# Performance work log

Measured on AMD Instinct MI355X. Metric: run time of the kernel, lower is better.

Reference implementation:

```python
import jax, jax.numpy as jnp
import numpy as np

B, F, H, M, T = 4096, 256, 256, 3, 30
IN0 = 2 + F  # GRU layer-0 input: concat(current_pos[2], context[F])


def setup_inputs() -> dict:
    key = jax.random.key(0)
    ks = jax.random.split(key, 15)
    s = 0.05
    rn = lambda k, shp: jax.random.normal(k, shp, jnp.float32) * s
    return dict(
        context=jax.random.normal(ks[0], (B, F), jnp.float32),
        mp_w1=rn(ks[1], (64, F)), mp_b1=rn(ks[2], (64,)),
        mp_w2=rn(ks[3], (M, 64)), mp_b2=rn(ks[4], (M,)),
        w_ih0=rn(ks[5], (M, 3 * H, IN0)), w_hh0=rn(ks[6], (M, 3 * H, H)),
        b_ih0=rn(ks[7], (M, 3 * H)), b_hh0=rn(ks[8], (M, 3 * H)),
        w_ih1=rn(ks[9], (M, 3 * H, H)), w_hh1=rn(ks[10], (M, 3 * H, H)),
        b_ih1=rn(ks[11], (M, 3 * H)), b_hh1=rn(ks[12], (M, 3 * H)),
        out_w=rn(ks[13], (M, 2, H)), out_b=rn(ks[14], (M, 2)),
        num_future_steps=T,
    )


def _gru_cell(x, h, w_ih, w_hh, b_ih, b_hh):
    # PyTorch GRU cell, gate order (r, z, n)
    gx = x @ w_ih.T + b_ih  # (B, 3H)
    gh = h @ w_hh.T + b_hh  # (B, 3H)
    xr, xz, xn = jnp.split(gx, 3, axis=-1)
    hr, hz, hn = jnp.split(gh, 3, axis=-1)
    r = jax.nn.sigmoid(xr + hr)
    z = jax.nn.sigmoid(xz + hz)
    n = jnp.tanh(xn + r * hn)
    return (1.0 - z) * n + z * h


def reference(context, mp_w1, mp_b1, mp_w2, mp_b2,
              w_ih0, w_hh0, b_ih0, b_hh0,
              w_ih1, w_hh1, b_ih1, b_hh1,
              out_w, out_b, num_future_steps):
    mode_logits = jax.nn.relu(context @ mp_w1.T + mp_b1) @ mp_w2.T + mp_b2
    mode_probs = jax.nn.softmax(mode_logits, axis=-1)  # (B, M)

    def decode_mode(wi0, wh0, bi0, bh0, wi1, wh1, bi1, bh1, ow, ob):
        def step(carry, _):
            h0, h1, pos = carry
            x = jnp.concatenate([pos, context], axis=-1)  # (B, 2+F)
            h0n = _gru_cell(x, h0, wi0, wh0, bi0, bh0)
            h1n = _gru_cell(h0n, h1, wi1, wh1, bi1, bh1)
            delta = h1n @ ow.T + ob  # (B, 2)
            return (h0n, h1n, delta), delta

        pos0 = jnp.zeros((context.shape[0], 2), context.dtype)
        # hidden = context.unsqueeze(0).repeat(2,1,1): both layers init to context
        (_, _, _), deltas = jax.lax.scan(step, (context, context, pos0), None,
                                          length=num_future_steps)
        # deltas: (T, B, 2) -> (B, T, 2), cumulative sum over time
        return jnp.cumsum(deltas.transpose(1, 0, 2), axis=1)

    trajs = jax.vmap(decode_mode)(w_ih0, w_hh0, b_ih0, b_hh0,
                                  w_ih1, w_hh1, b_ih1, b_hh1,
                                  out_w, out_b)  # (M, B, T, 2)
    trajectories = trajs.transpose(1, 0, 2, 3)  # (B, M, T, 2)
    return trajectories, mode_probs
```

## Files before the change

### kernel.cpp

```cpp
#include <hip/hip_runtime.h>


typedef __attribute__((ext_vector_type(8))) short bf16x8;
typedef __attribute__((ext_vector_type(4))) float f32x4;

__device__ __forceinline__ short f2bf(float f) {
    unsigned u = __builtin_bit_cast(unsigned, f);
    unsigned r = (u + 0x7fffu + ((u >> 16) & 1u)) >> 16;
    return (short)r;
}
__device__ __forceinline__ float bf2f(short s) {
    unsigned u = ((unsigned)(unsigned short)s) << 16;
    return __builtin_bit_cast(float, u);
}
__device__ __forceinline__ float fast_sigmoid(float x) {
    x = fminf(fmaxf(x, -30.f), 30.f);
    float e = __builtin_amdgcn_exp2f(x * -1.442695041f);
    return __builtin_amdgcn_rcpf(1.f + e);
}
__device__ __forceinline__ float fast_tanh(float x) {
    x = fminf(fmaxf(x, -15.f), 15.f);
    float e = __builtin_amdgcn_exp2f(x * -2.885390082f);
    return (1.f - e) * __builtin_amdgcn_rcpf(1.f + e);
}

__global__ void prep_kernel(const float* __restrict__ w_ih0,
                            const float* __restrict__ w_hh0,
                            const float* __restrict__ w_ih1,
                            const float* __restrict__ w_hh1,
                            short* __restrict__ ws) {
    int bid = blockIdx.x;
    int L = threadIdx.x;
    const float* src;
    int srcRowLen, colBase, m, w, ks, t;
    if (bid < 1152) {
        int idx = bid, mw = idx / 48, blk = idx % 48;
        m = mw / 8; w = mw % 8;
        if (blk < 32) { ks = blk >> 2; t = blk & 3; }
        else { int q = blk - 32; ks = q >> 1; t = 4 + (q & 1); }
        src = w_hh0 + (size_t)m * 768 * 256; srcRowLen = 256; colBase = 0;
    } else if (bid < 3456) {
        int idx = bid - 1152, mw = idx / 96, blk = idx % 96;
        m = mw / 8; w = mw % 8;
        int half;
        if (blk < 64) { half = blk >> 5; ks = (blk >> 2) & 7; t = blk & 3; }
        else { int q = blk - 64; half = q >> 4; ks = (q >> 1) & 7; t = 4 + (q & 1); }
        src = (half ? w_hh1 : w_ih1) + (size_t)m * 768 * 256;
        srcRowLen = 256; colBase = 0;
    } else {
        int idx = bid - 3456, mw = idx / 48, blk = idx % 48;
        m = mw / 8; w = mw % 8; ks = blk / 6; t = blk % 6;
        src = w_ih0 + (size_t)m * 768 * 258; srcRowLen = 258; colBase = 2;
    }
    int row = (t >> 1) * 256 + 32 * w + (t & 1) * 16 + (L & 15);
    int col0 = colBase + ks * 32 + (L >> 4) * 8;
    short* dst = ws + (size_t)bid * 512 + L * 8;
    const float* s = src + (size_t)row * srcRowLen + col0;
#pragma unroll
    for (int j = 0; j < 8; ++j) dst[j] = f2bf(s[j]);
}

__global__ __launch_bounds__(256) void modeprobs_kernel(
    const float* __restrict__ ctx, const float* __restrict__ w1,
    const float* __restrict__ b1, const float* __restrict__ w2,
    const float* __restrict__ b2, float* __restrict__ out,
    long probs_off) {
    __shared__ float w1s[64 * 256];
    int tid = threadIdx.x;
    int j = tid & 63;
    int rsub = tid >> 6;
#pragma unroll
    for (int i = 0; i < 64; ++i) w1s[tid + i * 256] = w1[tid + i * 256];
    float b1v = b1[j];
    float w2v0 = w2[j], w2v1 = w2[64 + j], w2v2 = w2[128 + j];
    float b20 = b2[0], b21 = b2[1], b22 = b2[2];
    __syncthreads();
    for (int c = 0; c < 16; ++c) {
        int brow = blockIdx.x * 64 + c * 4 + rsub;
        const float* crow = ctx + (size_t)brow * 256;
        float accv = b1v;
#pragma unroll 8
        for (int k = 0; k < 256; ++k) {
            int kk = (k + j) & 255;
            accv += w1s[j * 256 + kk] * crow[kk];
        }
        float h = fmaxf(accv, 0.f);
        float l0 = h * w2v0, l1 = h * w2v1, l2 = h * w2v2;
#pragma unroll
        for (int s = 1; s < 64; s <<= 1) {
            l0 += __shfl_xor(l0, s);
            l1 += __shfl_xor(l1, s);
            l2 += __shfl_xor(l2, s);
        }
        if (j == 0) {
            l0 += b20; l1 += b21; l2 += b22;
            float mx = fmaxf(l0, fmaxf(l1, l2));
            float e0 = __builtin_amdgcn_exp2f((l0 - mx) * 1.442695041f);
            float e1 = __builtin_amdgcn_exp2f((l1 - mx) * 1.442695041f);
            float e2 = __builtin_amdgcn_exp2f((l2 - mx) * 1.442695041f);
            float inv = 1.f / (e0 + e1 + e2);
            out[probs_off + (size_t)brow * 3 + 0] = e0 * inv;
            out[probs_off + (size_t)brow * 3 + 1] = e1 * inv;
            out[probs_off + (size_t)brow * 3 + 2] = e2 * inv;
        }
    }
}

__global__ __launch_bounds__(512, 2) void decoder_kernel(
    const float* __restrict__ context,
    const float* __restrict__ w_ih0_f,
    const float* __restrict__ b_ih0, const float* __restrict__ b_hh0,
    const float* __restrict__ b_ih1, const float* __restrict__ b_hh1,
    const float* __restrict__ out_w, const float* __restrict__ out_b,
    const short* __restrict__ ws, float* __restrict__ out,
    const int* __restrict__ pT, int ntiles) {
    __shared__ short ctxS[64 * 264];
    __shared__ short h0a[64 * 264], h0b[64 * 264];
    __shared__ short h1s[64 * 264];
    __shared__ float posD[128];
    __shared__ float owl[512];
    __shared__ float cwp0[768], cwp1[768];
    __shared__ float cbA[512];
    __shared__ float cbXn[256];
    __shared__ float cbh0n[256];
    __shared__ float cb1A[512];
    __shared__ float cb1X[256];
    __shared__ float cb1H[256];

    const int bid = blockIdx.x;
    const int xcd = bid & 7, slot = bid >> 3;
    int mode, xl, nx;
    if (xcd < 3)      { mode = 0; xl = xcd;     nx = 3; }
    else if (xcd < 6) { mode = 1; xl = xcd - 3; nx = 3; }
    else              { mode = 2; xl = xcd - 6; nx = 2; }
    const int g = slot * nx + xl;
    if (g >= ntiles) return;
    const int m = mode;
    const int b0 = g * 64;

    const int T = *pT;
    const int tid = threadIdx.x;
    const int lane = tid & 63, w = tid >> 6;
    const int lr = lane & 15, quad = lane >> 4;

    if (tid < 128) posD[tid] = 0.f;
    owl[tid] = out_w[m * 512 + tid];
    if (tid < 512) {
        cbA[tid] = b_ih0[m * 768 + tid] + b_hh0[m * 768 + tid];
        cb1A[tid] = b_ih1[m * 768 + tid] + b_hh1[m * 768 + tid];
    }
    if (tid < 256) {
        cbXn[tid] = b_ih0[m * 768 + 512 + tid];
        cbh0n[tid] = b_hh0[m * 768 + 512 + tid];
        cb1X[tid] = b_ih1[m * 768 + 512 + tid];
        cb1H[tid] = b_hh1[m * 768 + 512 + tid];
    }
    for (int c = tid; c < 768; c += 512) {
        cwp0[c] = w_ih0_f[((size_t)m * 768 + c) * 258 + 0];
        cwp1[c] = w_ih0_f[((size_t)m * 768 + c) * 258 + 1];
    }
#pragma unroll
    for (int i = 0; i < 32; ++i) {
        int idx = tid + i * 512;
        int r = idx >> 8, k = idx & 255;
        short v = f2bf(context[(size_t)(b0 + r) * 256 + k]);
        ctxS[r * 264 + k] = v;
        h0a[r * 264 + k] = v;
        h1s[r * 264 + k] = v;
    }
    const float ob0v = out_b[m * 2 + 0], ob1v = out_b[m * 2 + 1];

    const short* p0w = ws + ((size_t)(m * 8 + w) * 48) * 512 + lane * 8;
    const short* p1w = ws + (size_t)1152 * 512 + ((size_t)(m * 8 + w) * 96) * 512 + lane * 8;
    const short* pcw = ws + (size_t)3456 * 512 + ((size_t)(m * 8 + w) * 48) * 512 + lane * 8;

    const int cA = 32 * w + lr;
    const int cB = 32 * w + 16 + lr;

    __syncthreads();

    float cum0 = 0.f, cum1 = 0.f;

    for (int st = 0; st < T; ++st) {
        const short* h0c = (st & 1) ? h0b : h0a;
        short* h0n_ = (st & 1) ? h0a : h0b;

        {
            f32x4 arz[4][4], axn[2][4], ahn[2][4];
#pragma unroll
            for (int rt = 0; rt < 4; ++rt)
#pragma unroll
                for (int r = 0; r < 4; ++r) {
                    int row = rt * 16 + quad * 4 + r;
                    float px = posD[row * 2], py = posD[row * 2 + 1];
#pragma unroll
                    for (int t = 0; t < 4; ++t) {
                        int c = (t >> 1) * 256 + ((t & 1) ? cB : cA);
                        arz[t][rt][r] = cbA[c] + px * cwp0[c] + py * cwp1[c];
                    }
#pragma unroll
                    for (int nt = 0; nt < 2; ++nt) {
                        int cn = nt ? cB : cA;
                        axn[nt][rt][r] = cbXn[cn] + px * cwp0[512 + cn] +
                                         py * cwp1[512 + cn];
                        ahn[nt][rt][r] = cbh0n[cn];
                    }
                }
            const short* bpc = pcw;
            const short* bp0rz = p0w;
            const short* bp0n = p0w + 32 * 512;
#pragma unroll 1
            for (int ks = 0; ks < 8; ++ks) {
                bf16x8 ac[4], ah[4];
#pragma unroll
                for (int rt = 0; rt < 4; ++rt) {
                    ac[rt] = *reinterpret_cast<const bf16x8*>(
                        ctxS + (rt * 16 + lr) * 264 + ks * 32 + quad * 8);
                    ah[rt] = *reinterpret_cast<const bf16x8*>(
                        h0c + (rt * 16 + lr) * 264 + ks * 32 + quad * 8);
                }
#pragma unroll
                for (int t = 0; t < 4; ++t) {
                    bf16x8 b = *reinterpret_cast<const bf16x8*>(bpc + t * 512);
#pragma unroll
                    for (int rt = 0; rt < 4; ++rt)
                        arz[t][rt] = __builtin_amdgcn_mfma_f32_16x16x32_bf16(
                            ac[rt], b, arz[t][rt], 0, 0, 0);
                }
#pragma unroll
                for (int nt = 0; nt < 2; ++nt) {
                    bf16x8 b = *reinterpret_cast<const bf16x8*>(bpc + (4 + nt) * 512);
#pragma unroll
                    for (int rt = 0; rt < 4; ++rt)
                        axn[nt][rt] = __builtin_amdgcn_mfma_f32_16x16x32_bf16(
                            ac[rt], b, axn[nt][rt], 0, 0, 0);
                }
#pragma unroll
                for (int t = 0; t < 4; ++t) {
                    bf16x8 b = *reinterpret_cast<const bf16x8*>(bp0rz + t * 512);
#pragma unroll
                    for (int rt = 0; rt < 4; ++rt)
                        arz[t][rt] = __builtin_amdgcn_mfma_f32_16x16x32_bf16(
                            ah[rt], b, arz[t][rt], 0, 0, 0);
                }
#pragma unroll
                for (int nt = 0; nt < 2; ++nt) {
                    bf16x8 b = *reinterpret_cast<const bf16x8*>(bp0n + nt * 512);
#pragma unroll
                    for (int rt = 0; rt < 4; ++rt)
                        ahn[nt][rt] = __builtin_amdgcn_mfma_f32_16x16x32_bf16(
                            ah[rt], b, ahn[nt][rt], 0, 0, 0);
                }
                bpc += 6 * 512;
                bp0rz += 4 * 512;
                bp0n += 2 * 512;
            }
#pragma unroll
            for (int nt = 0; nt < 2; ++nt) {
                int col = nt ? cB : cA;
#pragma unroll
                for (int rt = 0; rt < 4; ++rt)
#pragma unroll
                    for (int r = 0; r < 4; ++r) {
                        int row = rt * 16 + quad * 4 + r;
                        float rr = fast_sigmoid(arz[nt][rt][r]);
                        float zz = fast_sigmoid(arz[2 + nt][rt][r]);
                        float nn =
                            fast_tanh(axn[nt][rt][r] + rr * ahn[nt][rt][r]);
                        float hold = bf2f(h0c[row * 264 + col]);
                        h0n_[row * 264 + col] = f2bf((1.f - zz) * nn + zz * hold);
                    }
            }
        }
        __syncthreads();

        {
            f32x4 arz[4][4], axn[2][4], ahn[2][4];
#pragma unroll
            for (int rt = 0; rt < 4; ++rt)
#pragma unroll
                for (int r = 0; r < 4; ++r) {
#pragma unroll
                    for (int t = 0; t < 4; ++t) {
                        int c = (t >> 1) * 256 + ((t & 1) ? cB : cA);
                        arz[t][rt][r] = cb1A[c];
                    }
#pragma unroll
                    for (int nt = 0; nt < 2; ++nt) {
                        int cn = nt ? cB : cA;
                        axn[nt][rt][r] = cb1X[cn];
                        ahn[nt][rt][r] = cb1H[cn];
                    }
                }
            const short* bq0 = p1w;
            const short* bq1 = p1w + 32 * 512;
            const short* bx = p1w + 64 * 512;
            const short* bh = p1w + 80 * 512;
#pragma unroll 1
            for (int ks = 0; ks < 8; ++ks) {
                bf16x8 a0[4], a1[4];
#pragma unroll
                for (int rt = 0; rt < 4; ++rt) {
                    a0[rt] = *reinterpret_cast<const bf16x8*>(
                        h0n_ + (rt * 16 + lr) * 264 + ks * 32 + quad * 8);
                    a1[rt] = *reinterpret_cast<const bf16x8*>(
                        h1s + (rt * 16 + lr) * 264 + ks * 32 + quad * 8);
                }
#pragma unroll
                for (int t = 0; t < 4; ++t) {
                    bf16x8 b = *reinterpret_cast<const bf16x8*>(bq0 + t * 512);
#pragma unroll
                    for (int rt = 0; rt < 4; ++rt)
                        arz[t][rt] = __builtin_amdgcn_mfma_f32_16x16x32_bf16(
                            a0[rt], b, arz[t][rt], 0, 0, 0);
                }
#pragma unroll
                for (int nt = 0; nt < 2; ++nt) {
                    bf16x8 b = *reinterpret_cast<const bf16x8*>(bx + nt * 512);
#pragma unroll
                    for (int rt = 0; rt < 4; ++rt)
                        axn[nt][rt] = __builtin_amdgcn_mfma_f32_16x16x32_bf16(
                            a0[rt], b, axn[nt][rt], 0, 0, 0);
                }
#pragma unroll
                for (int t = 0; t < 4; ++t) {
                    bf16x8 b = *reinterpret_cast<const bf16x8*>(bq1 + t * 512);
#pragma unroll
                    for (int rt = 0; rt < 4; ++rt)
                        arz[t][rt] = __builtin_amdgcn_mfma_f32_16x16x32_bf16(
                            a1[rt], b, arz[t][rt], 0, 0, 0);
                }
#pragma unroll
                for (int nt = 0; nt < 2; ++nt) {
                    bf16x8 b = *reinterpret_cast<const bf16x8*>(bh + nt * 512);
#pragma unroll
                    for (int rt = 0; rt < 4; ++rt)
                        ahn[nt][rt] = __builtin_amdgcn_mfma_f32_16x16x32_bf16(
                            a1[rt], b, ahn[nt][rt], 0, 0, 0);
                }
                bq0 += 4 * 512;
                bq1 += 4 * 512;
                bx += 2 * 512;
                bh += 2 * 512;
            }
            __syncthreads();
#pragma unroll
            for (int nt = 0; nt < 2; ++nt) {
                int col = nt ? cB : cA;
#pragma unroll
                for (int rt = 0; rt < 4; ++rt)
#pragma unroll
                    for (int r = 0; r < 4; ++r) {
                        int row = rt * 16 + quad * 4 + r;
                        float rr = fast_sigmoid(arz[nt][rt][r]);
                        float zz = fast_sigmoid(arz[2 + nt][rt][r]);
                        float nn =
                            fast_tanh(axn[nt][rt][r] + rr * ahn[nt][rt][r]);
                        float hold = bf2f(h1s[row * 264 + col]);
                        h1s[row * 264 + col] = f2bf((1.f - zz) * nn + zz * hold);
                    }
            }
        }
        __syncthreads();

        {
            int brow = tid >> 3, p = tid & 7;
            float d0 = 0.f, d1 = 0.f;
#pragma unroll
            for (int j = 0; j < 4; ++j) {
                int cb = ((p + brow) & 7) * 8 + j * 64;
                bf16x8 hv8 = *reinterpret_cast<const bf16x8*>(h1s + brow * 264 + cb);
#pragma unroll
                for (int i = 0; i < 8; ++i) {
                    float hv = bf2f(hv8[i]);
                    d0 += hv * owl[cb + i];
                    d1 += hv * owl[256 + cb + i];
                }
            }
            d0 += __shfl_xor(d0, 1); d0 += __shfl_xor(d0, 2); d0 += __shfl_xor(d0, 4);
            d1 += __shfl_xor(d1, 1); d1 += __shfl_xor(d1, 2); d1 += __shfl_xor(d1, 4);
            d0 += ob0v;
            d1 += ob1v;
            if (p == 0) {
                cum0 += d0;
                cum1 += d1;
                size_t o = (((size_t)(b0 + brow) * 3 + m) * (size_t)T + st) * 2;
                out[o] = cum0;
                out[o + 1] = cum1;
                posD[brow * 2] = d0;
                posD[brow * 2 + 1] = d1;
            }
        }
        __syncthreads();
    }
}

extern "C" void kernel_launch(void* const* d_in, const int* in_sizes, int n_in,
                              void* d_out, int out_size, void* d_ws, size_t ws_size,
                              hipStream_t stream) {
    const float* context = (const float*)d_in[0];
    const float* mp_w1 = (const float*)d_in[1];
    const float* mp_b1 = (const float*)d_in[2];
    const float* mp_w2 = (const float*)d_in[3];
    const float* mp_b2 = (const float*)d_in[4];
    const float* w_ih0 = (const float*)d_in[5];
    const float* w_hh0 = (const float*)d_in[6];
    const float* b_ih0 = (const float*)d_in[7];
    const float* b_hh0 = (const float*)d_in[8];
    const float* w_ih1 = (const float*)d_in[9];
    const float* w_hh1 = (const float*)d_in[10];
    const float* b_ih1 = (const float*)d_in[11];
    const float* b_hh1 = (const float*)d_in[12];
    const float* out_w = (const float*)d_in[13];
    const float* out_b = (const float*)d_in[14];
    const int* pT = (const int*)d_in[15];
    float* out = (float*)d_out;
    short* ws = (short*)d_ws;

    const int B = in_sizes[0] / 256;
    const int ntiles = B / 64;
    const long probs_off = (long)out_size - (long)B * 3;

    prep_kernel<<<4608, 64, 0, stream>>>(w_ih0, w_hh0, w_ih1, w_hh1, ws);
    modeprobs_kernel<<<B / 64, 256, 0, stream>>>(context, mp_w1, mp_b1, mp_w2,
                                                 mp_b2, out, probs_off);
    const int nslots = (ntiles + 1) / 2;
    decoder_kernel<<<8 * nslots, 512, 0, stream>>>(
        context, w_ih0, b_ih0, b_hh0, b_ih1, b_hh1, out_w, out_b, ws, out, pT,
        ntiles);
}
```

Before: 976.4 us.

## Double decoder block to 1024 threads, halving per-wave column tiles

The decoder block grows from 8 to 16 waves, so each wave computes one 16-column slice per gate instead of two, which cuts the accumulator registers per wave roughly in half. Weight pointers are rebased per half-wave with readfirstlane, and the output projection is re-partitioned to 16 lanes per row. Some bias and position-weight tables are stored in LDS as bf16 to save shared memory. In exchange each wave now reloads the same A tiles for fewer MFMAs, which doubles LDS read traffic per block, and the bf16 biases lose some precision.

```diff
diff --git a/kernel.cpp b/kernel.cpp
--- a/kernel.cpp
+++ b/kernel.cpp
@@ -106,7 +106,7 @@
     }
 }
 
-__global__ __launch_bounds__(512, 2) void decoder_kernel(
+__global__ __launch_bounds__(1024, 4) void decoder_kernel(
     const float* __restrict__ context,
     const float* __restrict__ w_ih0_f,
     const float* __restrict__ b_ih0, const float* __restrict__ b_hh0,
@@ -119,13 +119,11 @@
     __shared__ short h1s[64 * 264];
     __shared__ float posD[128];
     __shared__ float owl[512];
-    __shared__ float cwp0[768], cwp1[768];
+    __shared__ short cwp0h[768], cwp1h[768];
     __shared__ float cbA[512];
-    __shared__ float cbXn[256];
-    __shared__ float cbh0n[256];
     __shared__ float cb1A[512];
-    __shared__ float cb1X[256];
-    __shared__ float cb1H[256];
+    __shared__ short cbXn[256], cbh0n[256];
+    __shared__ short cb1X[256], cb1H[256];
 
     const int bid = blockIdx.x;
     const int xcd = bid & 7, slot = bid >> 3;
@@ -140,28 +138,30 @@
 
     const int T = *pT;
     const int tid = threadIdx.x;
-    const int lane = tid & 63, w = tid >> 6;
+    const int lane = tid & 63, wv = tid >> 6;
+    const int w8 = wv >> 1, hh = wv & 1;
     const int lr = lane & 15, quad = lane >> 4;
+    const int cA = 32 * w8 + 16 * hh + lr;
 
     if (tid < 128) posD[tid] = 0.f;
-    owl[tid] = out_w[m * 512 + tid];
     if (tid < 512) {
+        owl[tid] = out_w[m * 512 + tid];
         cbA[tid] = b_ih0[m * 768 + tid] + b_hh0[m * 768 + tid];
         cb1A[tid] = b_ih1[m * 768 + tid] + b_hh1[m * 768 + tid];
     }
     if (tid < 256) {
-        cbXn[tid] = b_ih0[m * 768 + 512 + tid];
-        cbh0n[tid] = b_hh0[m * 768 + 512 + tid];
-        cb1X[tid] = b_ih1[m * 768 + 512 + tid];
-        cb1H[tid] = b_hh1[m * 768 + 512 + tid];
-    }
-    for (int c = tid; c < 768; c += 512) {
-        cwp0[c] = w_ih0_f[((size_t)m * 768 + c) * 258 + 0];
-        cwp1[c] = w_ih0_f[((size_t)m * 768 + c) * 258 + 1];
-    }
-#pragma unroll
-    for (int i = 0; i < 32; ++i) {
-        int idx = tid + i * 512;
+        cbXn[tid] = f2bf(b_ih0[m * 768 + 512 + tid]);
+        cbh0n[tid] = f2bf(b_hh0[m * 768 + 512 + tid]);
+        cb1X[tid] = f2bf(b_ih1[m * 768 + 512 + tid]);
+        cb1H[tid] = f2bf(b_hh1[m * 768 + 512 + tid]);
+    }
+    if (tid < 768) {
+        cwp0h[tid] = f2bf(w_ih0_f[((size_t)m * 768 + tid) * 258 + 0]);
+        cwp1h[tid] = f2bf(w_ih0_f[((size_t)m * 768 + tid) * 258 + 1]);
+    }
+#pragma unroll
+    for (int i = 0; i < 16; ++i) {
+        int idx = tid + i * 1024;
         int r = idx >> 8, k = idx & 255;
         short v = f2bf(context[(size_t)(b0 + r) * 256 + k]);
         ctxS[r * 264 + k] = v;
@@ -170,12 +170,20 @@
     }
     const float ob0v = out_b[m * 2 + 0], ob1v = out_b[m * 2 + 1];
 
-    const short* p0w = ws + ((size_t)(m * 8 + w) * 48) * 512 + lane * 8;
-    const short* p1w = ws + (size_t)1152 * 512 + ((size_t)(m * 8 + w) * 96) * 512 + lane * 8;
-    const short* pcw = ws + (size_t)3456 * 512 + ((size_t)(m * 8 + w) * 48) * 512 + lane * 8;
-
-    const int cA = 32 * w + lr;
-    const int cB = 32 * w + 16 + lr;
+    const int base0 =
+        __builtin_amdgcn_readfirstlane(((m * 8 + w8) * 48 + hh) * 512);
+    const int base1 = __builtin_amdgcn_readfirstlane(
+        (1152 + (m * 8 + w8) * 96 + hh) * 512);
+    const int basec = __builtin_amdgcn_readfirstlane(
+        (3456 + (m * 8 + w8) * 48 + hh) * 512);
+    const short* pH = ws + base0;
+    const short* pHn = ws + base0 + 32 * 512;
+    const short* pI1 = ws + base1;
+    const short* pQ1 = ws + base1 + 32 * 512;
+    const short* pX1 = ws + base1 + 64 * 512;
+    const short* pN1 = ws + base1 + 80 * 512;
+    const short* pC = ws + basec;
+    const int lv = lane * 8;
 
     __syncthreads();
 
@@ -186,189 +194,179 @@
         short* h0n_ = (st & 1) ? h0a : h0b;
 
         {
-            f32x4 arz[4][4], axn[2][4], ahn[2][4];
+            f32x4 arz[2][4], axn[4], ahn[4];
+            const int cz = 256 + cA, cn = 512 + cA;
+            const float bAr = cbA[cA], bAz = cbA[cz];
+            const float w0r = bf2f(cwp0h[cA]), w1r = bf2f(cwp1h[cA]);
+            const float w0z = bf2f(cwp0h[cz]), w1z = bf2f(cwp1h[cz]);
+            const float w0n = bf2f(cwp0h[cn]), w1n = bf2f(cwp1h[cn]);
+            const float bXn = bf2f(cbXn[cA]), bHn = bf2f(cbh0n[cA]);
 #pragma unroll
             for (int rt = 0; rt < 4; ++rt)
 #pragma unroll
                 for (int r = 0; r < 4; ++r) {
                     int row = rt * 16 + quad * 4 + r;
                     float px = posD[row * 2], py = posD[row * 2 + 1];
-#pragma unroll
-                    for (int t = 0; t < 4; ++t) {
-                        int c = (t >> 1) * 256 + ((t & 1) ? cB : cA);
-                        arz[t][rt][r] = cbA[c] + px * cwp0[c] + py * cwp1[c];
-                    }
-#pragma unroll
-                    for (int nt = 0; nt < 2; ++nt) {
-                        int cn = nt ? cB : cA;
-                        axn[nt][rt][r] = cbXn[cn] + px * cwp0[512 + cn] +
-                                         py * cwp1[512 + cn];
-                        ahn[nt][rt][r] = cbh0n[cn];
-                    }
-                }
-            const short* bpc = pcw;
-            const short* bp0rz = p0w;
-            const short* bp0n = p0w + 32 * 512;
+                    arz[0][rt][r] = bAr + px * w0r + py * w1r;
+                    arz[1][rt][r] = bAz + px * w0z + py * w1z;
+                    axn[rt][r] = bXn + px * w0n + py * w1n;
+                    ahn[rt][r] = bHn;
+                }
+            const short* qC = pC;
+            const short* qH = pH;
+            const short* qHn = pHn;
 #pragma unroll 1
             for (int ks = 0; ks < 8; ++ks) {
-                bf16x8 ac[4], ah[4];
-#pragma unroll
-                for (int rt = 0; rt < 4; ++rt) {
-                    ac[rt] = *reinterpret_cast<const bf16x8*>(
-                        ctxS + (rt * 16 + lr) * 264 + ks * 32 + quad * 8);
-                    ah[rt] = *reinterpret_cast<const bf16x8*>(
-                        h0c + (rt * 16 + lr) * 264 + ks * 32 + quad * 8);
-                }
-#pragma unroll
-                for (int t = 0; t < 4; ++t) {
-                    bf16x8 b = *reinterpret_cast<const bf16x8*>(bpc + t * 512);
-#pragma unroll
-                    for (int rt = 0; rt < 4; ++rt)
-                        arz[t][rt] = __builtin_amdgcn_mfma_f32_16x16x32_bf16(
-                            ac[rt], b, arz[t][rt], 0, 0, 0);
-                }
-#pragma unroll
-                for (int nt = 0; nt < 2; ++nt) {
-                    bf16x8 b = *reinterpret_cast<const bf16x8*>(bpc + (4 + nt) * 512);
-#pragma unroll
-                    for (int rt = 0; rt < 4; ++rt)
-                        axn[nt][rt] = __builtin_amdgcn_mfma_f32_16x16x32_bf16(
-                            ac[rt], b, axn[nt][rt], 0, 0, 0);
-                }
-#pragma unroll
-                for (int t = 0; t < 4; ++t) {
-                    bf16x8 b = *reinterpret_cast<const bf16x8*>(bp0rz + t * 512);
-#pragma unroll
-                    for (int rt = 0; rt < 4; ++rt)
-                        arz[t][rt] = __builtin_amdgcn_mfma_f32_16x16x32_bf16(
-                            ah[rt], b, arz[t][rt], 0, 0, 0);
-                }
-#pragma unroll
-                for (int nt = 0; nt < 2; ++nt) {
-                    bf16x8 b = *reinterpret_cast<const bf16x8*>(bp0n + nt * 512);
-#pragma unroll
-                    for (int rt = 0; rt < 4; ++rt)
-                        ahn[nt][rt] = __builtin_amdgcn_mfma_f32_16x16x32_bf16(
-                            ah[rt], b, ahn[nt][rt], 0, 0, 0);
-                }
-                bpc += 6 * 512;
-                bp0rz += 4 * 512;
-                bp0n += 2 * 512;
+                bf16x8 a[4];
+                {
+                    bf16x8 b0 = *reinterpret_cast<const bf16x8*>(qC + lv);
+                    bf16x8 b1 = *reinterpret_cast<const bf16x8*>(qC + lv + 2 * 512);
+                    bf16x8 b2 = *reinterpret_cast<const bf16x8*>(qC + lv + 4 * 512);
+#pragma unroll
+                    for (int rt = 0; rt < 4; ++rt)
+                        a[rt] = *reinterpret_cast<const bf16x8*>(
+                            ctxS + (rt * 16 + lr) * 264 + ks * 32 + quad * 8);
+#pragma unroll
+                    for (int rt = 0; rt < 4; ++rt)
+                        arz[0][rt] = __builtin_amdgcn_mfma_f32_16x16x32_bf16(
+                            a[rt], b0, arz[0][rt], 0, 0, 0);
+#pragma unroll
+                    for (int rt = 0; rt < 4; ++rt)
+                        arz[1][rt] = __builtin_amdgcn_mfma_f32_16x16x32_bf16(
+                            a[rt], b1, arz[1][rt], 0, 0, 0);
+#pragma unroll
+                    for (int rt = 0; rt < 4; ++rt)
+                        axn[rt] = __builtin_amdgcn_mfma_f32_16x16x32_bf16(
+                            a[rt], b2, axn[rt], 0, 0, 0);
+                }
+                {
+                    bf16x8 c0 = *reinterpret_cast<const bf16x8*>(qH + lv);
+                    bf16x8 c1 = *reinterpret_cast<const bf16x8*>(qH + lv + 2 * 512);
+                    bf16x8 c2 = *reinterpret_cast<const bf16x8*>(qHn + lv);
+#pragma unroll
+                    for (int rt = 0; rt < 4; ++rt)
+                        a[rt] = *reinterpret_cast<const bf16x8*>(
+                            h0c + (rt * 16 + lr) * 264 + ks * 32 + quad * 8);
+#pragma unroll
+                    for (int rt = 0; rt < 4; ++rt)
+                        arz[0][rt] = __builtin_amdgcn_mfma_f32_16x16x32_bf16(
+                            a[rt], c0, arz[0][rt], 0, 0, 0);
+#pragma unroll
+                    for (int rt = 0; rt < 4; ++rt)
+                        arz[1][rt] = __builtin_amdgcn_mfma_f32_16x16x32_bf16(
+                            a[rt], c1, arz[1][rt], 0, 0, 0);
+#pragma unroll
+                    for (int rt = 0; rt < 4; ++rt)
+                        ahn[rt] = __builtin_amdgcn_mfma_f32_16x16x32_bf16(
+                            a[rt], c2, ahn[rt], 0, 0, 0);
+                }
+                qC += 6 * 512;
+                qH += 4 * 512;
+                qHn += 2 * 512;
             }
 #pragma unroll
-            for (int nt = 0; nt < 2; ++nt) {
-                int col = nt ? cB : cA;
-#pragma unroll
-                for (int rt = 0; rt < 4; ++rt)
-#pragma unroll
-                    for (int r = 0; r < 4; ++r) {
-                        int row = rt * 16 + quad * 4 + r;
-                        float rr = fast_sigmoid(arz[nt][rt][r]);
-                        float zz = fast_sigmoid(arz[2 + nt][rt][r]);
-                        float nn =
-                            fast_tanh(axn[nt][rt][r] + rr * ahn[nt][rt][r]);
-                        float hold = bf2f(h0c[row * 264 + col]);
-                        h0n_[row * 264 + col] = f2bf((1.f - zz) * nn + zz * hold);
-                    }
-            }
+            for (int rt = 0; rt < 4; ++rt)
+#pragma unroll
+                for (int r = 0; r < 4; ++r) {
+                    int row = rt * 16 + quad * 4 + r;
+                    float rr = fast_sigmoid(arz[0][rt][r]);
+                    float zz = fast_sigmoid(arz[1][rt][r]);
+                    float nn = fast_tanh(axn[rt][r] + rr * ahn[rt][r]);
+                    float hold = bf2f(h0c[row * 264 + cA]);
+                    h0n_[row * 264 + cA] = f2bf((1.f - zz) * nn + zz * hold);
+                }
         }
         __syncthreads();
 
         {
-            f32x4 arz[4][4], axn[2][4], ahn[2][4];
+            f32x4 arz[2][4], axn[4], ahn[4];
+            const int cz = 256 + cA;
+            const float bAr = cb1A[cA], bAz = cb1A[cz];
+            const float bXv = bf2f(cb1X[cA]), bHv = bf2f(cb1H[cA]);
 #pragma unroll
             for (int rt = 0; rt < 4; ++rt)
 #pragma unroll
                 for (int r = 0; r < 4; ++r) {
-#pragma unroll
-                    for (int t = 0; t < 4; ++t) {
-                        int c = (t >> 1) * 256 + ((t & 1) ? cB : cA);
-                        arz[t][rt][r] = cb1A[c];
-                    }
-#pragma unroll
-                    for (int nt = 0; nt < 2; ++nt) {
-                        int cn = nt ? cB : cA;
-                        axn[nt][rt][r] = cb1X[cn];
-                        ahn[nt][rt][r] = cb1H[cn];
-                    }
-                }
-            const short* bq0 = p1w;
-            const short* bq1 = p1w + 32 * 512;
-            const short* bx = p1w + 64 * 512;
-            const short* bh = p1w + 80 * 512;
+                    arz[0][rt][r] = bAr;
+                    arz[1][rt][r] = bAz;
+                    axn[rt][r] = bXv;
+                    ahn[rt][r] = bHv;
+                }
+            const short* qI = pI1;
+            const short* qQ = pQ1;
+            const short* qX = pX1;
+            const short* qN = pN1;
 #pragma unroll 1
             for (int ks = 0; ks < 8; ++ks) {
-                bf16x8 a0[4], a1[4];
-#pragma unroll
-                for (int rt = 0; rt < 4; ++rt) {
-                    a0[rt] = *reinterpret_cast<const bf16x8*>(
-                        h0n_ + (rt * 16 + lr) * 264 + ks * 32 + quad * 8);
-                    a1[rt] = *reinterpret_cast<const bf16x8*>(
-                        h1s + (rt * 16 + lr) * 264 + ks * 32 + quad * 8);
-                }
-#pragma unroll
-                for (int t = 0; t < 4; ++t) {
-                    bf16x8 b = *reinterpret_cast<const bf16x8*>(bq0 + t * 512);
-#pragma unroll
-                    for (int rt = 0; rt < 4; ++rt)
-                        arz[t][rt] = __builtin_amdgcn_mfma_f32_16x16x32_bf16(
-                            a0[rt], b, arz[t][rt], 0, 0, 0);
-                }
-#pragma unroll
-                for (int nt = 0; nt < 2; ++nt) {
-                    bf16x8 b = *reinterpret_cast<const bf16x8*>(bx + nt * 512);
-#pragma unroll
-                    for (int rt = 0; rt < 4; ++rt)
-                        axn[nt][rt] = __builtin_amdgcn_mfma_f32_16x16x32_bf16(
-                            a0[rt], b, axn[nt][rt], 0, 0, 0);
-                }
-#pragma unroll
-                for (int t = 0; t < 4; ++t) {
-                    bf16x8 b = *reinterpret_cast<const bf16x8*>(bq1 + t * 512);
-#pragma unroll
-                    for (int rt = 0; rt < 4; ++rt)
-                        arz[t][rt] = __builtin_amdgcn_mfma_f32_16x16x32_bf16(
-                            a1[rt], b, arz[t][rt], 0, 0, 0);
-                }
-#pragma unroll
-                for (int nt = 0; nt < 2; ++nt) {
-                    bf16x8 b = *reinterpret_cast<const bf16x8*>(bh + nt * 512);
-#pragma unroll
-                    for (int rt = 0; rt < 4; ++rt)
-                        ahn[nt][rt] = __builtin_amdgcn_mfma_f32_16x16x32_bf16(
-                            a1[rt], b, ahn[nt][rt], 0, 0, 0);
-                }
-                bq0 += 4 * 512;
-                bq1 += 4 * 512;
-                bx += 2 * 512;
-                bh += 2 * 512;
+                bf16x8 a[4];
+                {
+                    bf16x8 b0 = *reinterpret_cast<const bf16x8*>(qI + lv);
+                    bf16x8 b1 = *reinterpret_cast<const bf16x8*>(qI + lv + 2 * 512);
+                    bf16x8 b2 = *reinterpret_cast<const bf16x8*>(qX + lv);
+#pragma unroll
+                    for (int rt = 0; rt < 4; ++rt)
+                        a[rt] = *reinterpret_cast<const bf16x8*>(
+                            h0n_ + (rt * 16 + lr) * 264 + ks * 32 + quad * 8);
+#pragma unroll
+                    for (int rt = 0; rt < 4; ++rt)
+                        arz[0][rt] = __builtin_amdgcn_mfma_f32_16x16x32_bf16(
+                            a[rt], b0, arz[0][rt], 0, 0, 0);
+#pragma unroll
+                    for (int rt = 0; rt < 4; ++rt)
+                        arz[1][rt] = __builtin_amdgcn_mfma_f32_16x16x32_bf16(
+                            a[rt], b1, arz[1][rt], 0, 0, 0);
+#pragma unroll
+                    for (int rt = 0; rt < 4; ++rt)
+                        axn[rt] = __builtin_amdgcn_mfma_f32_16x16x32_bf16(
+                            a[rt], b2, axn[rt], 0, 0, 0);
+                }
+                {
+                    bf16x8 c0 = *reinterpret_cast<const bf16x8*>(qQ + lv);
+                    bf16x8 c1 = *reinterpret_cast<const bf16x8*>(qQ + lv + 2 * 512);
+                    bf16x8 c2 = *reinterpret_cast<const bf16x8*>(qN + lv);
+#pragma unroll
+                    for (int rt = 0; rt < 4; ++rt)
+                        a[rt] = *reinterpret_cast<const bf16x8*>(
+                            h1s + (rt * 16 + lr) * 264 + ks * 32 + quad * 8);
+#pragma unroll
+                    for (int rt = 0; rt < 4; ++rt)
+                        arz[0][rt] = __builtin_amdgcn_mfma_f32_16x16x32_bf16(
+                            a[rt], c0, arz[0][rt], 0, 0, 0);
+#pragma unroll
+                    for (int rt = 0; rt < 4; ++rt)
+                        arz[1][rt] = __builtin_amdgcn_mfma_f32_16x16x32_bf16(
+                            a[rt], c1, arz[1][rt], 0, 0, 0);
+#pragma unroll
+                    for (int rt = 0; rt < 4; ++rt)
+                        ahn[rt] = __builtin_amdgcn_mfma_f32_16x16x32_bf16(
+                            a[rt], c2, ahn[rt], 0, 0, 0);
+                }
+                qI += 4 * 512;
+                qQ += 4 * 512;
+                qX += 2 * 512;
+                qN += 2 * 512;
             }
             __syncthreads();
 #pragma unroll
-            for (int nt = 0; nt < 2; ++nt) {
-                int col = nt ? cB : cA;
-#pragma unroll
-                for (int rt = 0; rt < 4; ++rt)
-#pragma unroll
-                    for (int r = 0; r < 4; ++r) {
-                        int row = rt * 16 + quad * 4 + r;
-                        float rr = fast_sigmoid(arz[nt][rt][r]);
-                        float zz = fast_sigmoid(arz[2 + nt][rt][r]);
-                        float nn =
-                            fast_tanh(axn[nt][rt][r] + rr * ahn[nt][rt][r]);
-                        float hold = bf2f(h1s[row * 264 + col]);
-                        h1s[row * 264 + col] = f2bf((1.f - zz) * nn + zz * hold);
-                    }
-            }
+            for (int rt = 0; rt < 4; ++rt)
+#pragma unroll
+                for (int r = 0; r < 4; ++r) {
+                    int row = rt * 16 + quad * 4 + r;
+                    float rr = fast_sigmoid(arz[0][rt][r]);
+                    float zz = fast_sigmoid(arz[1][rt][r]);
+                    float nn = fast_tanh(axn[rt][r] + rr * ahn[rt][r]);
+                    float hold = bf2f(h1s[row * 264 + cA]);
+                    h1s[row * 264 + cA] = f2bf((1.f - zz) * nn + zz * hold);
+                }
         }
         __syncthreads();
 
         {
-            int brow = tid >> 3, p = tid & 7;
+            int brow = tid >> 4, p = tid & 15;
             float d0 = 0.f, d1 = 0.f;
 #pragma unroll
-            for (int j = 0; j < 4; ++j) {
-                int cb = ((p + brow) & 7) * 8 + j * 64;
+            for (int j = 0; j < 2; ++j) {
+                int cb = ((p + brow) & 15) * 16 + j * 8;
                 bf16x8 hv8 = *reinterpret_cast<const bf16x8*>(h1s + brow * 264 + cb);
 #pragma unroll
                 for (int i = 0; i < 8; ++i) {
@@ -377,8 +375,10 @@
                     d1 += hv * owl[256 + cb + i];
                 }
             }
-            d0 += __shfl_xor(d0, 1); d0 += __shfl_xor(d0, 2); d0 += __shfl_xor(d0, 4);
-            d1 += __shfl_xor(d1, 1); d1 += __shfl_xor(d1, 2); d1 += __shfl_xor(d1, 4);
+            d0 += __shfl_xor(d0, 1); d0 += __shfl_xor(d0, 2);
+            d0 += __shfl_xor(d0, 4); d0 += __shfl_xor(d0, 8);
+            d1 += __shfl_xor(d1, 1); d1 += __shfl_xor(d1, 2);
+            d1 += __shfl_xor(d1, 4); d1 += __shfl_xor(d1, 8);
             d0 += ob0v;
             d1 += ob1v;
             if (p == 0) {
@@ -425,7 +425,7 @@
     modeprobs_kernel<<<B / 64, 256, 0, stream>>>(context, mp_w1, mp_b1, mp_w2,
                                                  mp_b2, out, probs_off);
     const int nslots = (ntiles + 1) / 2;
-    decoder_kernel<<<8 * nslots, 512, 0, stream>>>(
+    decoder_kernel<<<8 * nslots, 1024, 0, stream>>>(
         context, w_ih0, b_ih0, b_hh0, b_ih1, b_hh1, out_w, out_b, ws, out, pT,
         ntiles);
 }
```

Result: slower. 1.338 ms (+37.0%).

## Precompute loop-invariant context input-gate projection once and reuse across timesteps

Applied to the files above, without the earlier changes.

Adds a decoder variant that computes the layer-0 input projection of the constant context (plus biases) once before the time loop and stores it as bf16 in global workspace. Each step then reloads these precomputed gate values, adds the rank-2 position term from cached weight columns, and runs only the hidden-state GEMM for layer 0. This removes a third of layer-0 MFMA work per step. In exchange it adds global memory traffic per step, an extra bf16 rounding of the context gates, and a fallback path when the workspace is too small.

```diff
diff --git a/kernel.cpp b/kernel.cpp
--- a/kernel.cpp
+++ b/kernel.cpp
@@ -2,6 +2,7 @@
 
 
 typedef __attribute__((ext_vector_type(8))) short bf16x8;
+typedef __attribute__((ext_vector_type(4))) short short4n;
 typedef __attribute__((ext_vector_type(4))) float f32x4;
 
 __device__ __forceinline__ short f2bf(float f) {
@@ -106,7 +107,358 @@
     }
 }
 
-__global__ __launch_bounds__(512, 2) void decoder_kernel(
+__global__ __launch_bounds__(512, 2) void decoder_gxc(
+    const float* __restrict__ context,
+    const float* __restrict__ w_ih0_f,
+    const float* __restrict__ b_ih0, const float* __restrict__ b_hh0,
+    const float* __restrict__ b_ih1, const float* __restrict__ b_hh1,
+    const float* __restrict__ out_w, const float* __restrict__ out_b,
+    short* ws, float* __restrict__ out,
+    const int* __restrict__ pT, int ntiles) {
+    __shared__ short h0a[64 * 264], h0b[64 * 264];
+    __shared__ short h1s[64 * 264];
+    __shared__ float posD[128];
+    __shared__ float owl[512];
+    __shared__ float cwp0[768], cwp1[768];
+    __shared__ float cbA[512];
+    __shared__ float cbXn[256];
+    __shared__ float cbh0n[256];
+    __shared__ float cb1A[512];
+    __shared__ float cb1X[256];
+    __shared__ float cb1H[256];
+
+    const int bid = blockIdx.x;
+    const int xcd = bid & 7, slot = bid >> 3;
+    int mode, xl, nx;
+    if (xcd < 3)      { mode = 0; xl = xcd;     nx = 3; }
+    else if (xcd < 6) { mode = 1; xl = xcd - 3; nx = 3; }
+    else              { mode = 2; xl = xcd - 6; nx = 2; }
+    const int g = slot * nx + xl;
+    if (g >= ntiles) return;
+    const int m = mode;
+    const int b0 = g * 64;
+    const int wk = m * ntiles + g;
+
+    const int T = *pT;
+    const int tid = threadIdx.x;
+    const int lane = tid & 63, w = tid >> 6;
+    const int lr = lane & 15, quad = lane >> 4;
+
+    if (tid < 128) posD[tid] = 0.f;
+    owl[tid] = out_w[m * 512 + tid];
+    if (tid < 512) {
+        cbA[tid] = b_ih0[m * 768 + tid] + b_hh0[m * 768 + tid];
+        cb1A[tid] = b_ih1[m * 768 + tid] + b_hh1[m * 768 + tid];
+    }
+    if (tid < 256) {
+        cbXn[tid] = b_ih0[m * 768 + 512 + tid];
+        cbh0n[tid] = b_hh0[m * 768 + 512 + tid];
+        cb1X[tid] = b_ih1[m * 768 + 512 + tid];
+        cb1H[tid] = b_hh1[m * 768 + 512 + tid];
+    }
+    for (int cc = tid; cc < 768; cc += 512) {
+        cwp0[cc] = w_ih0_f[((size_t)m * 768 + cc) * 258 + 0];
+        cwp1[cc] = w_ih0_f[((size_t)m * 768 + cc) * 258 + 1];
+    }
+#pragma unroll
+    for (int i = 0; i < 32; ++i) {
+        int idx = tid + i * 512;
+        int r = idx >> 8, k = idx & 255;
+        short v = f2bf(context[(size_t)(b0 + r) * 256 + k]);
+        h0a[r * 264 + k] = v;
+        h1s[r * 264 + k] = v;
+    }
+    const float ob0v = out_b[m * 2 + 0], ob1v = out_b[m * 2 + 1];
+
+    const short* p0w = ws + ((size_t)(m * 8 + w) * 48) * 512 + lane * 8;
+    const short* p1w = ws + (size_t)1152 * 512 + ((size_t)(m * 8 + w) * 96) * 512 + lane * 8;
+    const short* pcw = ws + (size_t)3456 * 512 + ((size_t)(m * 8 + w) * 48) * 512 + lane * 8;
+
+    short* gxw = ws + (size_t)4608 * 512 +
+                 ((size_t)(wk * 8 + w) * 24) * 256 + lane * 4;
+
+    const int cA = 32 * w + lr;
+    const int cB = 32 * w + 16 + lr;
+
+    __syncthreads();
+
+    {
+        f32x4 arz[4][4], axn[2][4];
+#pragma unroll
+        for (int rt = 0; rt < 4; ++rt)
+#pragma unroll
+            for (int r = 0; r < 4; ++r) {
+#pragma unroll
+                for (int t = 0; t < 4; ++t) {
+                    int c = (t >> 1) * 256 + ((t & 1) ? cB : cA);
+                    arz[t][rt][r] = cbA[c];
+                }
+#pragma unroll
+                for (int nt = 0; nt < 2; ++nt)
+                    axn[nt][rt][r] = cbXn[nt ? cB : cA];
+            }
+        const short* bpc = pcw;
+#pragma unroll 1
+        for (int ks = 0; ks < 8; ++ks) {
+            bf16x8 ac[4];
+#pragma unroll
+            for (int rt = 0; rt < 4; ++rt)
+                ac[rt] = *reinterpret_cast<const bf16x8*>(
+                    h0a + (rt * 16 + lr) * 264 + ks * 32 + quad * 8);
+#pragma unroll
+            for (int t = 0; t < 4; ++t) {
+                bf16x8 b = *reinterpret_cast<const bf16x8*>(bpc + t * 512);
+#pragma unroll
+                for (int rt = 0; rt < 4; ++rt)
+                    arz[t][rt] = __builtin_amdgcn_mfma_f32_16x16x32_bf16(
+                        ac[rt], b, arz[t][rt], 0, 0, 0);
+            }
+#pragma unroll
+            for (int nt = 0; nt < 2; ++nt) {
+                bf16x8 b = *reinterpret_cast<const bf16x8*>(bpc + (4 + nt) * 512);
+#pragma unroll
+                for (int rt = 0; rt < 4; ++rt)
+                    axn[nt][rt] = __builtin_amdgcn_mfma_f32_16x16x32_bf16(
+                        ac[rt], b, axn[nt][rt], 0, 0, 0);
+            }
+            bpc += 6 * 512;
+        }
+#pragma unroll
+        for (int t = 0; t < 4; ++t)
+#pragma unroll
+            for (int rt = 0; rt < 4; ++rt) {
+                short4n pk;
+#pragma unroll
+                for (int r = 0; r < 4; ++r) pk[r] = f2bf(arz[t][rt][r]);
+                *reinterpret_cast<short4n*>(gxw + (t * 4 + rt) * 256) = pk;
+            }
+#pragma unroll
+        for (int nt = 0; nt < 2; ++nt)
+#pragma unroll
+            for (int rt = 0; rt < 4; ++rt) {
+                short4n pk;
+#pragma unroll
+                for (int r = 0; r < 4; ++r) pk[r] = f2bf(axn[nt][rt][r]);
+                *reinterpret_cast<short4n*>(gxw + (16 + nt * 4 + rt) * 256) = pk;
+            }
+        asm volatile("s_waitcnt vmcnt(0)" ::: "memory");
+    }
+
+    float cum0 = 0.f, cum1 = 0.f;
+
+    for (int st = 0; st < T; ++st) {
+        const short* h0c = (st & 1) ? h0b : h0a;
+        short* h0n_ = (st & 1) ? h0a : h0b;
+
+        {
+            int gxo = 0;
+            asm volatile("" : "+v"(gxo));
+            const short* gq = gxw + gxo;
+
+            f32x4 arz[4][4], axn[2][4], ahn[2][4];
+#pragma unroll
+            for (int t = 0; t < 4; ++t) {
+                const int c = (t >> 1) * 256 + ((t & 1) ? cB : cA);
+                const float w0 = cwp0[c], w1 = cwp1[c];
+#pragma unroll
+                for (int rt = 0; rt < 4; ++rt) {
+                    short4n v = *reinterpret_cast<const short4n*>(
+                        gq + (t * 4 + rt) * 256);
+#pragma unroll
+                    for (int r = 0; r < 4; ++r) {
+                        int row = rt * 16 + quad * 4 + r;
+                        arz[t][rt][r] = bf2f(v[r]) + posD[row * 2] * w0 +
+                                        posD[row * 2 + 1] * w1;
+                    }
+                }
+            }
+#pragma unroll
+            for (int nt = 0; nt < 2; ++nt) {
+                const int cn = nt ? cB : cA;
+                const float w0 = cwp0[512 + cn], w1 = cwp1[512 + cn];
+                const float bh = cbh0n[cn];
+#pragma unroll
+                for (int rt = 0; rt < 4; ++rt) {
+                    short4n v = *reinterpret_cast<const short4n*>(
+                        gq + (16 + nt * 4 + rt) * 256);
+#pragma unroll
+                    for (int r = 0; r < 4; ++r) {
+                        int row = rt * 16 + quad * 4 + r;
+                        axn[nt][rt][r] = bf2f(v[r]) + posD[row * 2] * w0 +
+                                         posD[row * 2 + 1] * w1;
+                        ahn[nt][rt][r] = bh;
+                    }
+                }
+            }
+            const short* b0r = p0w;
+            const short* b0n = p0w + 32 * 512;
+#pragma unroll 1
+            for (int ks = 0; ks < 8; ++ks) {
+                bf16x8 ah[4];
+#pragma unroll
+                for (int rt = 0; rt < 4; ++rt)
+                    ah[rt] = *reinterpret_cast<const bf16x8*>(
+                        h0c + (rt * 16 + lr) * 264 + ks * 32 + quad * 8);
+#pragma unroll
+                for (int t = 0; t < 4; ++t) {
+                    bf16x8 b = *reinterpret_cast<const bf16x8*>(b0r + t * 512);
+#pragma unroll
+                    for (int rt = 0; rt < 4; ++rt)
+                        arz[t][rt] = __builtin_amdgcn_mfma_f32_16x16x32_bf16(
+                            ah[rt], b, arz[t][rt], 0, 0, 0);
+                }
+#pragma unroll
+                for (int nt = 0; nt < 2; ++nt) {
+                    bf16x8 b = *reinterpret_cast<const bf16x8*>(b0n + nt * 512);
+#pragma unroll
+                    for (int rt = 0; rt < 4; ++rt)
+                        ahn[nt][rt] = __builtin_amdgcn_mfma_f32_16x16x32_bf16(
+                            ah[rt], b, ahn[nt][rt], 0, 0, 0);
+                }
+                b0r += 4 * 512;
+                b0n += 2 * 512;
+            }
+#pragma unroll
+            for (int nt = 0; nt < 2; ++nt) {
+                int col = nt ? cB : cA;
+#pragma unroll
+                for (int rt = 0; rt < 4; ++rt)
+#pragma unroll
+                    for (int r = 0; r < 4; ++r) {
+                        int row = rt * 16 + quad * 4 + r;
+                        float rr = fast_sigmoid(arz[nt][rt][r]);
+                        float zz = fast_sigmoid(arz[2 + nt][rt][r]);
+                        float nn =
+                            fast_tanh(axn[nt][rt][r] + rr * ahn[nt][rt][r]);
+                        float hold = bf2f(h0c[row * 264 + col]);
+                        h0n_[row * 264 + col] = f2bf((1.f - zz) * nn + zz * hold);
+                    }
+            }
+        }
+        __syncthreads();
+
+        {
+            f32x4 arz[4][4], axn[2][4], ahn[2][4];
+#pragma unroll
+            for (int rt = 0; rt < 4; ++rt)
+#pragma unroll
+                for (int r = 0; r < 4; ++r) {
+#pragma unroll
+                    for (int t = 0; t < 4; ++t) {
+                        int c = (t >> 1) * 256 + ((t & 1) ? cB : cA);
+                        arz[t][rt][r] = cb1A[c];
+                    }
+#pragma unroll
+                    for (int nt = 0; nt < 2; ++nt) {
+                        int cn = nt ? cB : cA;
+                        axn[nt][rt][r] = cb1X[cn];
+                        ahn[nt][rt][r] = cb1H[cn];
+                    }
+                }
+            const short* bq0 = p1w;
+            const short* bq1 = p1w + 32 * 512;
+            const short* bx = p1w + 64 * 512;
+            const short* bh = p1w + 80 * 512;
+#pragma unroll 1
+            for (int ks = 0; ks < 8; ++ks) {
+                bf16x8 a0[4], a1[4];
+#pragma unroll
+                for (int rt = 0; rt < 4; ++rt) {
+                    a0[rt] = *reinterpret_cast<const bf16x8*>(
+                        h0n_ + (rt * 16 + lr) * 264 + ks * 32 + quad * 8);
+                    a1[rt] = *reinterpret_cast<const bf16x8*>(
+                        h1s + (rt * 16 + lr) * 264 + ks * 32 + quad * 8);
+                }
+#pragma unroll
+                for (int t = 0; t < 4; ++t) {
+                    bf16x8 b = *reinterpret_cast<const bf16x8*>(bq0 + t * 512);
+#pragma unroll
+                    for (int rt = 0; rt < 4; ++rt)
+                        arz[t][rt] = __builtin_amdgcn_mfma_f32_16x16x32_bf16(
+                            a0[rt], b, arz[t][rt], 0, 0, 0);
+                }
+#pragma unroll
+                for (int nt = 0; nt < 2; ++nt) {
+                    bf16x8 b = *reinterpret_cast<const bf16x8*>(bx + nt * 512);
+#pragma unroll
+                    for (int rt = 0; rt < 4; ++rt)
+                        axn[nt][rt] = __builtin_amdgcn_mfma_f32_16x16x32_bf16(
+                            a0[rt], b, axn[nt][rt], 0, 0, 0);
+                }
+#pragma unroll
+                for (int t = 0; t < 4; ++t) {
+                    bf16x8 b = *reinterpret_cast<const bf16x8*>(bq1 + t * 512);
+#pragma unroll
+                    for (int rt = 0; rt < 4; ++rt)
+                        arz[t][rt] = __builtin_amdgcn_mfma_f32_16x16x32_bf16(
+                            a1[rt], b, arz[t][rt], 0, 0, 0);
+                }
+#pragma unroll
+                for (int nt = 0; nt < 2; ++nt) {
+                    bf16x8 b = *reinterpret_cast<const bf16x8*>(bh + nt * 512);
+#pragma unroll
+                    for (int rt = 0; rt < 4; ++rt)
+                        ahn[nt][rt] = __builtin_amdgcn_mfma_f32_16x16x32_bf16(
+                            a1[rt], b, ahn[nt][rt], 0, 0, 0);
+                }
+                bq0 += 4 * 512;
+                bq1 += 4 * 512;
+                bx += 2 * 512;
+                bh += 2 * 512;
+            }
+            __syncthreads();
+#pragma unroll
+            for (int nt = 0; nt < 2; ++nt) {
+                int col = nt ? cB : cA;
+#pragma unroll
+                for (int rt = 0; rt < 4; ++rt)
+#pragma unroll
+                    for (int r = 0; r < 4; ++r) {
+                        int row = rt * 16 + quad * 4 + r;
+                        float rr = fast_sigmoid(arz[nt][rt][r]);
+                        float zz = fast_sigmoid(arz[2 + nt][rt][r]);
+                        float nn =
+                            fast_tanh(axn[nt][rt][r] + rr * ahn[nt][rt][r]);
+                        float hold = bf2f(h1s[row * 264 + col]);
+                        h1s[row * 264 + col] = f2bf((1.f - zz) * nn + zz * hold);
+                    }
+            }
+        }
+        __syncthreads();
+
+        {
+            int brow = tid >> 3, p = tid & 7;
+            float d0 = 0.f, d1 = 0.f;
+#pragma unroll
+            for (int j = 0; j < 4; ++j) {
+                int cb = ((p + brow) & 7) * 8 + j * 64;
+                bf16x8 hv8 = *reinterpret_cast<const bf16x8*>(h1s + brow * 264 + cb);
+#pragma unroll
+                for (int i = 0; i < 8; ++i) {
+                    float hv = bf2f(hv8[i]);
+                    d0 += hv * owl[cb + i];
+                    d1 += hv * owl[256 + cb + i];
+                }
+            }
+            d0 += __shfl_xor(d0, 1); d0 += __shfl_xor(d0, 2); d0 += __shfl_xor(d0, 4);
+            d1 += __shfl_xor(d1, 1); d1 += __shfl_xor(d1, 2); d1 += __shfl_xor(d1, 4);
+            d0 += ob0v;
+            d1 += ob1v;
+            if (p == 0) {
+                cum0 += d0;
+                cum1 += d1;
+                size_t o = (((size_t)(b0 + brow) * 3 + m) * (size_t)T + st) * 2;
+                out[o] = cum0;
+                out[o + 1] = cum1;
+                posD[brow * 2] = d0;
+                posD[brow * 2 + 1] = d1;
+            }
+        }
+        __syncthreads();
+    }
+}
+
+__global__ __launch_bounds__(512, 2) void decoder_base(
     const float* __restrict__ context,
     const float* __restrict__ w_ih0_f,
     const float* __restrict__ b_ih0, const float* __restrict__ b_hh0,
@@ -425,7 +777,16 @@
     modeprobs_kernel<<<B / 64, 256, 0, stream>>>(context, mp_w1, mp_b1, mp_w2,
                                                  mp_b2, out, probs_off);
     const int nslots = (ntiles + 1) / 2;
-    decoder_kernel<<<8 * nslots, 512, 0, stream>>>(
-        context, w_ih0, b_ih0, b_hh0, b_ih1, b_hh1, out_w, out_b, ws, out, pT,
-        ntiles);
-}
+
+    const size_t needed =
+        ((size_t)4608 * 512 + (size_t)3 * ntiles * 8 * 24 * 256) * sizeof(short);
+    if (ws_size >= needed) {
+        decoder_gxc<<<8 * nslots, 512, 0, stream>>>(
+            context, w_ih0, b_ih0, b_hh0, b_ih1, b_hh1, out_w, out_b, ws, out,
+            pT, ntiles);
+    } else {
+        decoder_base<<<8 * nslots, 512, 0, stream>>>(
+            context, w_ih0, b_ih0, b_hh0, b_ih1, b_hh1, out_w, out_b, ws, out,
+            pT, ntiles);
+    }
+}
```

Result: slower. 1.109 ms (+13.6%).
